# Performance work log

Hardware: AMD Instinct MI355X
Metric: run time of the kernel (lower is better)

## Reference

```python
import jax, jax.numpy as jnp
import numpy as np

B, CIN, COUT = 16, 64, 64
H, W = 96, 96
HK, AK = 3, 3  # hidden_kernels, attn_kernels


def setup_inputs() -> dict:
    key = jax.random.key(0)
    k1, k2, k3, k4, k5 = jax.random.split(key, 5)
    s = 1.0 / np.sqrt(CIN * HK * HK)
    return {
        "x1": jax.random.normal(k1, (B, CIN, H, W), jnp.float32),
        "x2": jax.random.normal(k2, (B, CIN, H, W), jnp.float32),
        "w1": jax.random.normal(k3, (COUT, CIN, HK, HK), jnp.float32) * s,
        "w2": jax.random.normal(k4, (COUT, CIN, HK, HK), jnp.float32) * s,
        "w3": jax.random.normal(k5, (COUT, CIN, HK, HK), jnp.float32) * s,
    }


def _conv(x, w):
    p = HK // 2
    return jax.lax.conv_general_dilated(x, w, (1, 1), [(p, p), (p, p)])


def _unfold_strided(x):
    # nn.Unfold(AK, stride=AK): non-overlapping AK x AK patches.
    # [B,C,H,W] -> [B, C*AK*AK, (H//AK)*(W//AK)], channel order (C, kh, kw).
    b, c, h, w = x.shape
    hp, wp = h // AK, w // AK
    x = x.reshape(b, c, hp, AK, wp, AK).transpose(0, 1, 3, 5, 2, 4)
    return x.reshape(b, c * AK * AK, hp * wp)


def _unfold_padded(x):
    # nn.Unfold(AK, padding=AK//2): stride-1 patches, output length H*W (AK odd).
    b, c, h, w = x.shape
    p = AK // 2
    xp = jnp.pad(x, ((0, 0), (0, 0), (p, p), (p, p)))
    cols = [xp[:, :, i:i + h, j:j + w] for i in range(AK) for j in range(AK)]
    return jnp.stack(cols, axis=2).reshape(b, c * AK * AK, h * w)


def reference(x1, x2, w1, w2, w3):
    aa = AK * AK
    L = (H // AK) * (W // AK)
    kf = _conv(x1, w1)   # [B, Cout, H, W]
    qf = _conv(x2, w2)
    vf = _conv(x1, w3)
    # key: [B, aa, Cout, L]; query: [B, aa, L, Cout]
    key = _unfold_strided(kf).reshape(B, COUT, aa, L).transpose(0, 2, 1, 3)
    qry = _unfold_strided(qf).reshape(B, COUT, aa, L).transpose(0, 2, 3, 1)
    # scores[b,k,c,d] over patches -> [B, aa, Cout_k, Cout_q]
    scores = jnp.einsum('bkcl,bkld->bkcd', key, qry)
    # transpose(1,3).flatten(2): [B, Cout_q, Cout_k*aa]
    scores = scores.transpose(0, 3, 2, 1).reshape(B, COUT, COUT * aa)
    scores = scores / np.sqrt(COUT * aa).astype(np.float32)
    attn = jax.nn.softmax(scores, axis=2)  # dynamic conv kernels
    vcols = _unfold_padded(vf)             # [B, Cout*aa, H*W]
    out = jnp.einsum('bce,bel->bcl', attn, vcols)
    return out.reshape(B, COUT, H, W)
```

## Files before the change

kernel.cpp:

```cpp
#include <hip/hip_runtime.h>


typedef __attribute__((ext_vector_type(8))) short short8v;
typedef __attribute__((ext_vector_type(4))) float floatx4;
typedef __attribute__((ext_vector_type(4))) unsigned int uint4v;

constexpr int PLANE = 9216;
constexpr int SC_F = 589824;

__device__ __forceinline__ unsigned short f2bf(float f) {
    unsigned int u = __float_as_uint(f);
    u = (u + 0x7FFFu + ((u >> 16) & 1u)) >> 16;
    return (unsigned short)u;
}
__device__ __forceinline__ float bf2f(unsigned short h) {
    return __uint_as_float(((unsigned int)h) << 16);
}

__global__ __launch_bounds__(256) void nchw2nhwc_bf16(
    const float* __restrict__ x, unsigned short* __restrict__ xh)
{
    int blk = blockIdx.x;
    int b = blk / 96, y = blk - b * 96;
    __shared__ float ls[64][96];
    const float* xp = x + (size_t)b * 64 * PLANE + (size_t)y * 96;
    for (int i = threadIdx.x; i < 64 * 96; i += 256) {
        int ci = i / 96, xc = i - ci * 96;
        ls[ci][xc] = xp[(size_t)ci * PLANE + xc];
    }
    __syncthreads();
    unsigned short* op = xh + ((size_t)b * PLANE + (size_t)y * 96) * 64;
    for (int i = threadIdx.x; i < 96 * 8; i += 256) {
        int xc = i >> 3, cg = i & 7;
        unsigned short tmp[8] __attribute__((aligned(16)));
        #pragma unroll
        for (int j = 0; j < 8; ++j) tmp[j] = f2bf(ls[cg * 8 + j][xc]);
        *(uint4v*)&op[(size_t)xc * 64 + cg * 8] = *(const uint4v*)tmp;
    }
}

__global__ __launch_bounds__(256) void wreorder(
    const float* __restrict__ w1, const float* __restrict__ w2,
    const float* __restrict__ w3, unsigned short* __restrict__ wl)
{
    int blk = blockIdx.x;
    int wi = blk / 9, k9 = blk - wi * 9;
    const float* w = (wi == 0) ? w1 : ((wi == 1) ? w2 : w3);
    unsigned short* o = wl + (size_t)wi * 9 * 4096 + (size_t)k9 * 4096;
    for (int i = threadIdx.x; i < 4096; i += 256)
        o[i] = f2bf(w[(size_t)i * 9 + k9]);
}

__global__ __launch_bounds__(256) void conv_mfma(
    const unsigned short* __restrict__ xh,
    const unsigned short* __restrict__ wl,
    void* __restrict__ out, int omode, int dynb)
{
    int blk = blockIdx.x;
    int xs3 = blk % 3; int t = blk / 3;
    int yq = t % 24;   int b = t / 24;
    int x0 = xs3 * 32, y0 = yq * 4;

    __shared__ __align__(16) unsigned short xs[6][34][72];

    const unsigned short* xb = xh + (size_t)b * PLANE * 64;
    for (int i = threadIdx.x; i < 6 * 34 * 8; i += 256) {
        int cg = i & 7, pix = i >> 3;
        int pr = pix / 34, pc = pix - pr * 34;
        int y = y0 - 1 + pr, x = x0 - 1 + pc;
        uint4v v = {0u, 0u, 0u, 0u};
        if ((unsigned)y < 96u && (unsigned)x < 96u)
            v = *(const uint4v*)&xb[((size_t)y * 96 + x) * 64 + cg * 8];
        *(uint4v*)&xs[pr][pc][cg * 8] = v;
    }
    __syncthreads();

    int lane = threadIdx.x & 63;
    int w = threadIdx.x >> 6;
    int ln = lane & 15, quad = lane >> 4;

    const unsigned short* wb = wl + (dynb ? (size_t)b * 9 * 4096 : 0);

    floatx4 acc[8];
    #pragma unroll
    for (int i = 0; i < 8; ++i) acc[i] = (floatx4){0.f, 0.f, 0.f, 0.f};

    #pragma unroll
    for (int k9 = 0; k9 < 9; ++k9) {
        int dy = k9 / 3, dx = k9 - dy * 3;
        #pragma unroll
        for (int ch = 0; ch < 2; ++ch) {
            short8v a = *(const short8v*)
                &wb[((size_t)k9 * 64 + (w * 16 + ln)) * 64 + ch * 32 + quad * 8];
            #pragma unroll
            for (int nt = 0; nt < 8; ++nt) {
                int n = nt * 16 + ln;
                int r = n >> 5, c = n & 31;
                short8v bf = *(const short8v*)
                    &xs[r + dy][c + dx][ch * 32 + quad * 8];
                acc[nt] = __builtin_amdgcn_mfma_f32_16x16x32_bf16(a, bf, acc[nt], 0, 0, 0);
            }
        }
    }

    #pragma unroll
    for (int nt = 0; nt < 8; ++nt) {
        int n = nt * 16 + ln;
        int r = n >> 5, c = n & 31;
        int y = y0 + r, x = x0 + c;
        if (omode == 2) {
            float* o = (float*)out;
            #pragma unroll
            for (int reg = 0; reg < 4; ++reg) {
                int co = w * 16 + quad * 4 + reg;
                o[((size_t)(b * 64 + co)) * PLANE + (size_t)y * 96 + x] = acc[nt][reg];
            }
        } else if (omode == 0) {
            unsigned short* o = (unsigned short*)out;
            #pragma unroll
            for (int reg = 0; reg < 4; ++reg) {
                int co = w * 16 + quad * 4 + reg;
                o[((size_t)(b * 64 + co)) * PLANE + (size_t)y * 96 + x] = f2bf(acc[nt][reg]);
            }
        } else {
            unsigned short* o = (unsigned short*)out;
            unsigned short tmp[4] __attribute__((aligned(8)));
            #pragma unroll
            for (int reg = 0; reg < 4; ++reg) tmp[reg] = f2bf(acc[nt][reg]);
            *(uint2*)&o[((size_t)b * PLANE + (size_t)y * 96 + x) * 64 + w * 16 + quad * 4]
                = *(const uint2*)tmp;
        }
    }
}

__global__ __launch_bounds__(256) void scores_kernel(
    const unsigned short* __restrict__ kf, const unsigned short* __restrict__ qf,
    float* __restrict__ scp, int nseg)
{
    int blk = blockIdx.x;
    int seg = blk % nseg;
    int bk  = blk / nseg;
    int b = bk / 9, k = bk - b * 9;
    int kh = k / 3, kw = k - kh * 3;

    __shared__ __align__(16) float Kt[64][68];
    __shared__ __align__(16) float Qt[64][68];

    const unsigned short* kb = kf + (size_t)b * 64 * PLANE;
    const unsigned short* qb = qf + (size_t)b * 64 * PLANE;
    int tc = threadIdx.x >> 4, td = threadIdx.x & 15;

    float acc[4][4] = {};
    int lcnt = 1024 / nseg;
    int lstart = seg * lcnt;
    for (int l0 = lstart; l0 < lstart + lcnt; l0 += 64) {
        __syncthreads();
        for (int i = threadIdx.x; i < 4096; i += 256) {
            int ch = i >> 6, ll = i & 63;
            int l = l0 + ll;
            int py = l >> 5, px = l & 31;
            int y = 3 * py + kh, xx = 3 * px + kw;
            Kt[ch][ll] = bf2f(kb[(size_t)ch * PLANE + y * 96 + xx]);
            Qt[ch][ll] = bf2f(qb[(size_t)ch * PLANE + y * 96 + xx]);
        }
        __syncthreads();
        #pragma unroll 4
        for (int ll = 0; ll < 64; ll += 4) {
            float4 kv[4], qv[4];
            #pragma unroll
            for (int i = 0; i < 4; ++i) kv[i] = *(const float4*)&Kt[tc * 4 + i][ll];
            #pragma unroll
            for (int j = 0; j < 4; ++j) qv[j] = *(const float4*)&Qt[td * 4 + j][ll];
            #pragma unroll
            for (int i = 0; i < 4; ++i)
                #pragma unroll
                for (int j = 0; j < 4; ++j)
                    acc[i][j] += kv[i].x * qv[j].x + kv[i].y * qv[j].y
                               + kv[i].z * qv[j].z + kv[i].w * qv[j].w;
        }
    }
    #pragma unroll
    for (int i = 0; i < 4; ++i)
        #pragma unroll
        for (int j = 0; j < 4; ++j) {
            int c = tc * 4 + i, d = td * 4 + j;
            scp[(size_t)seg * SC_F + (size_t)(b * 64 + d) * 576 + c * 9 + k] = acc[i][j];
        }
}

__global__ __launch_bounds__(64) void softmax_kernel(
    const float* __restrict__ sc, unsigned short* __restrict__ dynw, int nseg)
{
    int row = blockIdx.x;
    int lane = threadIdx.x;
    size_t base = (size_t)row * 576 + lane;
    float v[9];
    float mx = -3.0e38f;
    #pragma unroll
    for (int i = 0; i < 9; ++i) {
        float s = sc[base + i * 64];
        for (int g = 1; g < nseg; ++g) s += sc[(size_t)g * SC_F + base + i * 64];
        v[i] = s * (1.0f / 24.0f);
        mx = fmaxf(mx, v[i]);
    }
    #pragma unroll
    for (int o = 32; o; o >>= 1) mx = fmaxf(mx, __shfl_down(mx, o));
    mx = __shfl(mx, 0);
    float sum = 0.f;
    #pragma unroll
    for (int i = 0; i < 9; ++i) { v[i] = __expf(v[i] - mx); sum += v[i]; }
    #pragma unroll
    for (int o = 32; o; o >>= 1) sum += __shfl_down(sum, o);
    sum = __shfl(sum, 0);
    float inv = 1.0f / sum;
    int b = row >> 6, d = row & 63;
    #pragma unroll
    for (int i = 0; i < 9; ++i) {
        int e = i * 64 + lane;
        int c = e / 9, k = e - c * 9;
        dynw[(((size_t)b * 9 + k) * 64 + d) * 64 + c] = f2bf(v[i] * inv);
    }
}

extern "C" void kernel_launch(void* const* d_in, const int* in_sizes, int n_in,
                              void* d_out, int out_size, void* d_ws, size_t ws_size,
                              hipStream_t stream) {
    (void)in_sizes; (void)n_in; (void)out_size;
    const float* x1 = (const float*)d_in[0];
    const float* x2 = (const float*)d_in[1];
    const float* w1 = (const float*)d_in[2];
    const float* w2 = (const float*)d_in[3];
    const float* w3 = (const float*)d_in[4];
    float* out = (float*)d_out;

    char* ws = (char*)d_ws;
    constexpr size_t XHB = (size_t)16 * PLANE * 64 * 2;
    unsigned short* xh1 = (unsigned short*)(ws);
    unsigned short* xh2 = (unsigned short*)(ws + XHB);
    unsigned short* kf  = (unsigned short*)(ws + 2 * XHB);
    unsigned short* qf  = (unsigned short*)(ws + 3 * XHB);
    unsigned short* wl  = (unsigned short*)(ws + 4 * XHB);
    unsigned short* dynw = (unsigned short*)(ws + 4 * XHB + 221184);
    float* sc = (float*)(ws + 4 * XHB + 221184 + 1179648);

    size_t base = 4 * XHB + 221184 + 1179648;
    int nseg = (ws_size >= base + 4 * (size_t)SC_F * 4) ? 4 : 1;

    nchw2nhwc_bf16<<<dim3(1536), dim3(256), 0, stream>>>(x1, xh1);
    nchw2nhwc_bf16<<<dim3(1536), dim3(256), 0, stream>>>(x2, xh2);
    wreorder<<<dim3(27), dim3(256), 0, stream>>>(w1, w2, w3, wl);

    conv_mfma<<<dim3(1152), dim3(256), 0, stream>>>(xh1, wl,            kf, 0, 0);
    conv_mfma<<<dim3(1152), dim3(256), 0, stream>>>(xh2, wl + 9 * 4096, qf, 0, 0);
    scores_kernel<<<dim3(144 * nseg), dim3(256), 0, stream>>>(kf, qf, sc, nseg);
    softmax_kernel<<<dim3(1024), dim3(64), 0, stream>>>(sc, dynw, nseg);
    conv_mfma<<<dim3(1152), dim3(256), 0, stream>>>(xh1, wl + 18 * 4096, xh2, 1, 0);
    conv_mfma<<<dim3(1152), dim3(256), 0, stream>>>(xh2, dynw, out, 2, 1);
}
```

Before: 287.8 us.

## Use MFMA for scores, enlarge conv tiles with swizzled LDS, write patch-major K/Q

The conv kernel now computes an 8-row tile per block, with each wave handling 32 output channels across two MFMA accumulators, and its shared-memory tile uses an XOR swizzle to cut bank conflicts. The K and Q convs write their outputs straight into a patch-major [b,k9,c,l] layout. This lets a new MFMA-based scores kernel read contiguous bf16 rows instead of gathering strided scalars into fp32 LDS. Softmax packs four rows per block, and the split-L count drops from 4 to 2. The trade-off is higher register pressure from the doubled accumulators and scattered stores from the conv epilogue.

```diff
diff --git a/kernel.cpp b/kernel.cpp
--- a/kernel.cpp
+++ b/kernel.cpp
@@ -6,15 +6,12 @@
 typedef __attribute__((ext_vector_type(4))) unsigned int uint4v;
 
 constexpr int PLANE = 9216;
-constexpr int SC_F = 589824;
+constexpr int SCP_STRIDE = 589824;
 
 __device__ __forceinline__ unsigned short f2bf(float f) {
     unsigned int u = __float_as_uint(f);
     u = (u + 0x7FFFu + ((u >> 16) & 1u)) >> 16;
     return (unsigned short)u;
-}
-__device__ __forceinline__ float bf2f(unsigned short h) {
-    return __uint_as_float(((unsigned int)h) << 16);
 }
 
 __global__ __launch_bounds__(256) void nchw2nhwc_bf16(
@@ -58,47 +55,56 @@
 {
     int blk = blockIdx.x;
     int xs3 = blk % 3; int t = blk / 3;
-    int yq = t % 24;   int b = t / 24;
-    int x0 = xs3 * 32, y0 = yq * 4;
-
-    __shared__ __align__(16) unsigned short xs[6][34][72];
+    int yq = t % 12;   int b = t / 12;
+    int x0 = xs3 * 32, y0 = yq * 8;
+
+    __shared__ __align__(16) unsigned short xs[10 * 34 * 64];
 
     const unsigned short* xb = xh + (size_t)b * PLANE * 64;
-    for (int i = threadIdx.x; i < 6 * 34 * 8; i += 256) {
-        int cg = i & 7, pix = i >> 3;
+    for (int i = threadIdx.x; i < 2720; i += 256) {
+        int g = i & 7, pix = i >> 3;
         int pr = pix / 34, pc = pix - pr * 34;
         int y = y0 - 1 + pr, x = x0 - 1 + pc;
         uint4v v = {0u, 0u, 0u, 0u};
         if ((unsigned)y < 96u && (unsigned)x < 96u)
-            v = *(const uint4v*)&xb[((size_t)y * 96 + x) * 64 + cg * 8];
-        *(uint4v*)&xs[pr][pc][cg * 8] = v;
+            v = *(const uint4v*)&xb[((size_t)y * 96 + x) * 64 + g * 8];
+        *(uint4v*)&xs[pix * 64 + (g ^ (pc & 7)) * 8] = v;
     }
     __syncthreads();
 
     int lane = threadIdx.x & 63;
     int w = threadIdx.x >> 6;
     int ln = lane & 15, quad = lane >> 4;
+    int coh  = (w & 1) * 32;
+    int rowh = (w >> 1) * 4;
 
     const unsigned short* wb = wl + (dynb ? (size_t)b * 9 * 4096 : 0);
 
-    floatx4 acc[8];
-    #pragma unroll
-    for (int i = 0; i < 8; ++i) acc[i] = (floatx4){0.f, 0.f, 0.f, 0.f};
+    floatx4 acc[2][8];
+    #pragma unroll
+    for (int mi = 0; mi < 2; ++mi)
+        #pragma unroll
+        for (int nt = 0; nt < 8; ++nt) acc[mi][nt] = (floatx4){0.f, 0.f, 0.f, 0.f};
 
     #pragma unroll
     for (int k9 = 0; k9 < 9; ++k9) {
         int dy = k9 / 3, dx = k9 - dy * 3;
         #pragma unroll
         for (int ch = 0; ch < 2; ++ch) {
-            short8v a = *(const short8v*)
-                &wb[((size_t)k9 * 64 + (w * 16 + ln)) * 64 + ch * 32 + quad * 8];
+            short8v a0 = *(const short8v*)
+                &wb[((size_t)k9 * 64 + coh + ln) * 64 + ch * 32 + quad * 8];
+            short8v a1 = *(const short8v*)
+                &wb[((size_t)k9 * 64 + coh + 16 + ln) * 64 + ch * 32 + quad * 8];
+            int gb = ch * 4 + quad;
             #pragma unroll
             for (int nt = 0; nt < 8; ++nt) {
                 int n = nt * 16 + ln;
-                int r = n >> 5, c = n & 31;
+                int r = rowh + (n >> 5) + dy;
+                int c = (n & 31) + dx;
                 short8v bf = *(const short8v*)
-                    &xs[r + dy][c + dx][ch * 32 + quad * 8];
-                acc[nt] = __builtin_amdgcn_mfma_f32_16x16x32_bf16(a, bf, acc[nt], 0, 0, 0);
+                    &xs[(r * 34 + c) * 64 + (gb ^ (c & 7)) * 8];
+                acc[0][nt] = __builtin_amdgcn_mfma_f32_16x16x32_bf16(a0, bf, acc[0][nt], 0, 0, 0);
+                acc[1][nt] = __builtin_amdgcn_mfma_f32_16x16x32_bf16(a1, bf, acc[1][nt], 0, 0, 0);
             }
         }
     }
@@ -106,120 +112,126 @@
     #pragma unroll
     for (int nt = 0; nt < 8; ++nt) {
         int n = nt * 16 + ln;
-        int r = n >> 5, c = n & 31;
-        int y = y0 + r, x = x0 + c;
+        int y = y0 + rowh + (n >> 5), x = x0 + (n & 31);
         if (omode == 2) {
             float* o = (float*)out;
             #pragma unroll
-            for (int reg = 0; reg < 4; ++reg) {
-                int co = w * 16 + quad * 4 + reg;
-                o[((size_t)(b * 64 + co)) * PLANE + (size_t)y * 96 + x] = acc[nt][reg];
-            }
-        } else if (omode == 0) {
+            for (int mi = 0; mi < 2; ++mi)
+                #pragma unroll
+                for (int reg = 0; reg < 4; ++reg) {
+                    int co = coh + mi * 16 + quad * 4 + reg;
+                    o[((size_t)(b * 64 + co)) * PLANE + (size_t)y * 96 + x] = acc[mi][nt][reg];
+                }
+        } else if (omode == 1) {
             unsigned short* o = (unsigned short*)out;
             #pragma unroll
-            for (int reg = 0; reg < 4; ++reg) {
-                int co = w * 16 + quad * 4 + reg;
-                o[((size_t)(b * 64 + co)) * PLANE + (size_t)y * 96 + x] = f2bf(acc[nt][reg]);
+            for (int mi = 0; mi < 2; ++mi) {
+                unsigned short tmp[4] __attribute__((aligned(8)));
+                #pragma unroll
+                for (int reg = 0; reg < 4; ++reg) tmp[reg] = f2bf(acc[mi][nt][reg]);
+                *(uint2*)&o[((size_t)b * PLANE + (size_t)y * 96 + x) * 64 + coh + mi * 16 + quad * 4]
+                    = *(const uint2*)tmp;
             }
         } else {
             unsigned short* o = (unsigned short*)out;
-            unsigned short tmp[4] __attribute__((aligned(8)));
-            #pragma unroll
-            for (int reg = 0; reg < 4; ++reg) tmp[reg] = f2bf(acc[nt][reg]);
-            *(uint2*)&o[((size_t)b * PLANE + (size_t)y * 96 + x) * 64 + w * 16 + quad * 4]
-                = *(const uint2*)tmp;
+            int k9 = (y % 3) * 3 + (x % 3);
+            int l = (y / 3) * 32 + (x / 3);
+            #pragma unroll
+            for (int mi = 0; mi < 2; ++mi)
+                #pragma unroll
+                for (int reg = 0; reg < 4; ++reg) {
+                    int co = coh + mi * 16 + quad * 4 + reg;
+                    o[((size_t)(b * 9 + k9) * 64 + co) * 1024 + l] = f2bf(acc[mi][nt][reg]);
+                }
         }
     }
 }
 
-__global__ __launch_bounds__(256) void scores_kernel(
-    const unsigned short* __restrict__ kf, const unsigned short* __restrict__ qf,
+__global__ __launch_bounds__(256) void scores_mfma(
+    const unsigned short* __restrict__ kfc, const unsigned short* __restrict__ qfc,
     float* __restrict__ scp, int nseg)
 {
     int blk = blockIdx.x;
     int seg = blk % nseg;
     int bk  = blk / nseg;
-    int b = bk / 9, k = bk - b * 9;
-    int kh = k / 3, kw = k - kh * 3;
-
-    __shared__ __align__(16) float Kt[64][68];
-    __shared__ __align__(16) float Qt[64][68];
-
-    const unsigned short* kb = kf + (size_t)b * 64 * PLANE;
-    const unsigned short* qb = qf + (size_t)b * 64 * PLANE;
-    int tc = threadIdx.x >> 4, td = threadIdx.x & 15;
-
-    float acc[4][4] = {};
-    int lcnt = 1024 / nseg;
-    int lstart = seg * lcnt;
-    for (int l0 = lstart; l0 < lstart + lcnt; l0 += 64) {
-        __syncthreads();
-        for (int i = threadIdx.x; i < 4096; i += 256) {
-            int ch = i >> 6, ll = i & 63;
-            int l = l0 + ll;
-            int py = l >> 5, px = l & 31;
-            int y = 3 * py + kh, xx = 3 * px + kw;
-            Kt[ch][ll] = bf2f(kb[(size_t)ch * PLANE + y * 96 + xx]);
-            Qt[ch][ll] = bf2f(qb[(size_t)ch * PLANE + y * 96 + xx]);
-        }
-        __syncthreads();
-        #pragma unroll 4
-        for (int ll = 0; ll < 64; ll += 4) {
-            float4 kv[4], qv[4];
-            #pragma unroll
-            for (int i = 0; i < 4; ++i) kv[i] = *(const float4*)&Kt[tc * 4 + i][ll];
-            #pragma unroll
-            for (int j = 0; j < 4; ++j) qv[j] = *(const float4*)&Qt[td * 4 + j][ll];
-            #pragma unroll
-            for (int i = 0; i < 4; ++i)
-                #pragma unroll
-                for (int j = 0; j < 4; ++j)
-                    acc[i][j] += kv[i].x * qv[j].x + kv[i].y * qv[j].y
-                               + kv[i].z * qv[j].z + kv[i].w * qv[j].w;
-        }
-    }
+    int lane = threadIdx.x & 63, w = threadIdx.x >> 6;
+    int ln = lane & 15, quad = lane >> 4;
+    const unsigned short* ka = kfc + (size_t)bk * 64 * 1024;
+    const unsigned short* qa = qfc + (size_t)bk * 64 * 1024;
+
+    int Kblk = 1024 / nseg;
+    int Kw   = Kblk / 4;
+    int nch  = Kw / 32;
+
+    floatx4 acc[4][4];
     #pragma unroll
     for (int i = 0; i < 4; ++i)
         #pragma unroll
-        for (int j = 0; j < 4; ++j) {
-            int c = tc * 4 + i, d = td * 4 + j;
-            scp[(size_t)seg * SC_F + (size_t)(b * 64 + d) * 576 + c * 9 + k] = acc[i][j];
-        }
-}
-
-__global__ __launch_bounds__(64) void softmax_kernel(
-    const float* __restrict__ sc, unsigned short* __restrict__ dynw, int nseg)
-{
-    int row = blockIdx.x;
-    int lane = threadIdx.x;
-    size_t base = (size_t)row * 576 + lane;
+        for (int j = 0; j < 4; ++j) acc[i][j] = (floatx4){0.f, 0.f, 0.f, 0.f};
+
+    for (int chk = 0; chk < nch; ++chk) {
+        int l = seg * Kblk + w * Kw + chk * 32 + quad * 8;
+        short8v a[4], bq[4];
+        #pragma unroll
+        for (int mi = 0; mi < 4; ++mi)
+            a[mi] = *(const short8v*)&ka[(size_t)(mi * 16 + ln) * 1024 + l];
+        #pragma unroll
+        for (int ni = 0; ni < 4; ++ni)
+            bq[ni] = *(const short8v*)&qa[(size_t)(ni * 16 + ln) * 1024 + l];
+        #pragma unroll
+        for (int mi = 0; mi < 4; ++mi)
+            #pragma unroll
+            for (int ni = 0; ni < 4; ++ni)
+                acc[mi][ni] = __builtin_amdgcn_mfma_f32_16x16x32_bf16(a[mi], bq[ni], acc[mi][ni], 0, 0, 0);
+    }
+
+    __shared__ float ls[4][64][65];
+    #pragma unroll
+    for (int mi = 0; mi < 4; ++mi)
+        #pragma unroll
+        for (int ni = 0; ni < 4; ++ni)
+            #pragma unroll
+            for (int reg = 0; reg < 4; ++reg)
+                ls[w][ni * 16 + ln][mi * 16 + quad * 4 + reg] = acc[mi][ni][reg];
+    __syncthreads();
+
+    float* op = scp + (size_t)seg * SCP_STRIDE + (size_t)bk * 4096;
+    int t = threadIdx.x;
+    #pragma unroll
+    for (int j = 0; j < 16; ++j) {
+        int e = t * 16 + j;
+        int d = e >> 6, c = e & 63;
+        op[e] = ls[0][d][c] + ls[1][d][c] + ls[2][d][c] + ls[3][d][c];
+    }
+}
+
+__global__ __launch_bounds__(256) void softmax_kernel(
+    const float* __restrict__ scp, unsigned short* __restrict__ dynw, int nseg)
+{
+    int w = threadIdx.x >> 6, c = threadIdx.x & 63;
+    int row = blockIdx.x * 4 + w;
+    int b = row >> 6, d = row & 63;
     float v[9];
     float mx = -3.0e38f;
     #pragma unroll
-    for (int i = 0; i < 9; ++i) {
-        float s = sc[base + i * 64];
-        for (int g = 1; g < nseg; ++g) s += sc[(size_t)g * SC_F + base + i * 64];
-        v[i] = s * (1.0f / 24.0f);
-        mx = fmaxf(mx, v[i]);
-    }
-    #pragma unroll
-    for (int o = 32; o; o >>= 1) mx = fmaxf(mx, __shfl_down(mx, o));
-    mx = __shfl(mx, 0);
+    for (int k = 0; k < 9; ++k) {
+        size_t idx = (size_t)(b * 9 + k) * 4096 + d * 64 + c;
+        float s = scp[idx];
+        for (int g = 1; g < nseg; ++g) s += scp[(size_t)g * SCP_STRIDE + idx];
+        v[k] = s * (1.0f / 24.0f);
+        mx = fmaxf(mx, v[k]);
+    }
+    #pragma unroll
+    for (int o = 32; o; o >>= 1) mx = fmaxf(mx, __shfl_xor(mx, o));
     float sum = 0.f;
     #pragma unroll
-    for (int i = 0; i < 9; ++i) { v[i] = __expf(v[i] - mx); sum += v[i]; }
-    #pragma unroll
-    for (int o = 32; o; o >>= 1) sum += __shfl_down(sum, o);
-    sum = __shfl(sum, 0);
+    for (int k = 0; k < 9; ++k) { v[k] = __expf(v[k] - mx); sum += v[k]; }
+    #pragma unroll
+    for (int o = 32; o; o >>= 1) sum += __shfl_xor(sum, o);
     float inv = 1.0f / sum;
-    int b = row >> 6, d = row & 63;
-    #pragma unroll
-    for (int i = 0; i < 9; ++i) {
-        int e = i * 64 + lane;
-        int c = e / 9, k = e - c * 9;
-        dynw[(((size_t)b * 9 + k) * 64 + d) * 64 + c] = f2bf(v[i] * inv);
-    }
+    #pragma unroll
+    for (int k = 0; k < 9; ++k)
+        dynw[((size_t)(b * 9 + k) * 64 + d) * 64 + c] = f2bf(v[k] * inv);
 }
 
 extern "C" void kernel_launch(void* const* d_in, const int* in_sizes, int n_in,
@@ -237,23 +249,23 @@
     constexpr size_t XHB = (size_t)16 * PLANE * 64 * 2;
     unsigned short* xh1 = (unsigned short*)(ws);
     unsigned short* xh2 = (unsigned short*)(ws + XHB);
-    unsigned short* kf  = (unsigned short*)(ws + 2 * XHB);
-    unsigned short* qf  = (unsigned short*)(ws + 3 * XHB);
+    unsigned short* kfc = (unsigned short*)(ws + 2 * XHB);
+    unsigned short* qfc = (unsigned short*)(ws + 3 * XHB);
     unsigned short* wl  = (unsigned short*)(ws + 4 * XHB);
     unsigned short* dynw = (unsigned short*)(ws + 4 * XHB + 221184);
-    float* sc = (float*)(ws + 4 * XHB + 221184 + 1179648);
+    float* scp = (float*)(ws + 4 * XHB + 221184 + 1179648);
 
     size_t base = 4 * XHB + 221184 + 1179648;
-    int nseg = (ws_size >= base + 4 * (size_t)SC_F * 4) ? 4 : 1;
+    int nseg = (ws_size >= base + 2 * (size_t)SCP_STRIDE * 4) ? 2 : 1;
 
     nchw2nhwc_bf16<<<dim3(1536), dim3(256), 0, stream>>>(x1, xh1);
     nchw2nhwc_bf16<<<dim3(1536), dim3(256), 0, stream>>>(x2, xh2);
     wreorder<<<dim3(27), dim3(256), 0, stream>>>(w1, w2, w3, wl);
 
-    conv_mfma<<<dim3(1152), dim3(256), 0, stream>>>(xh1, wl,            kf, 0, 0);
-    conv_mfma<<<dim3(1152), dim3(256), 0, stream>>>(xh2, wl + 9 * 4096, qf, 0, 0);
-    scores_kernel<<<dim3(144 * nseg), dim3(256), 0, stream>>>(kf, qf, sc, nseg);
-    softmax_kernel<<<dim3(1024), dim3(64), 0, stream>>>(sc, dynw, nseg);
-    conv_mfma<<<dim3(1152), dim3(256), 0, stream>>>(xh1, wl + 18 * 4096, xh2, 1, 0);
-    conv_mfma<<<dim3(1152), dim3(256), 0, stream>>>(xh2, dynw, out, 2, 1);
-}
+    conv_mfma<<<dim3(576), dim3(256), 0, stream>>>(xh1, wl,            kfc, 3, 0);
+    conv_mfma<<<dim3(576), dim3(256), 0, stream>>>(xh2, wl + 9 * 4096, qfc, 3, 0);
+    scores_mfma<<<dim3(144 * nseg), dim3(256), 0, stream>>>(kfc, qfc, scp, nseg);
+    softmax_kernel<<<dim3(256), dim3(256), 0, stream>>>(scp, dynw, nseg);
+    conv_mfma<<<dim3(576), dim3(256), 0, stream>>>(xh1, wl + 18 * 4096, xh2, 1, 0);
+    conv_mfma<<<dim3(576), dim3(256), 0, stream>>>(xh2, dynw, out, 2, 1);
+}
```

After: 286.9 us. Within noise of the previous version (-0.3%).
